# Performance work log

Hardware: AMD Instinct MI355X
Metric: run time of the kernel (lower is better)

Reference implementation:

```python
import jax, jax.numpy as jnp
import numpy as np
import math

D_MODEL = 256
H = 8
D_K = D_MODEL // H
POS_OFFSET = 20
GRID = 7  # module hard-codes key_padding_mask.view(bs, 7, 7)


def _sine_pos_table(num_pos_feats=D_MODEL // 2, temperature=10000, rng=(-20, 20)):
    # faithful port of position_embedding_sine with normalize=True
    scale = 2 * math.pi
    emb = np.arange(rng[0], rng[1] + 1, dtype=np.float32)
    emb = emb / (emb[-1] + 1e-6) * scale  # normalize by last element (=20)
    dim_t = np.arange(num_pos_feats, dtype=np.float32)
    dim_t = temperature ** (2.0 * np.floor(dim_t / 2.0) / num_pos_feats)
    pos = emb[:, None] / dim_t  # [41, 128]
    pos = np.stack((np.sin(pos[:, 0::2]), np.cos(pos[:, 1::2])), axis=-1).reshape(pos.shape[0], -1)
    return jnp.asarray(pos, dtype=jnp.float32)  # [41, 128]


def setup_inputs() -> dict:
    key = jax.random.key(0)
    ks = jax.random.split(key, 8)
    L, B, D = 49, 2048, D_MODEL
    query = jax.random.normal(ks[0], (L, B, D), dtype=jnp.float32)
    key_t = jax.random.normal(ks[1], (L, B, D), dtype=jnp.float32)
    value = jax.random.normal(ks[2], (L, B, D), dtype=jnp.float32)
    key_padding_mask = jnp.zeros((B, L), dtype=bool)  # no padding
    # parameters (xavier-ish init)
    lim = math.sqrt(6.0 / (3 * D + D))
    in_proj_weight = jax.random.uniform(ks[3], (3 * D, D), minval=-lim, maxval=lim, dtype=jnp.float32)
    in_proj_bias = jnp.zeros((3 * D,), dtype=jnp.float32)
    out_w = jax.random.uniform(ks[4], (D, D), minval=-1.0 / math.sqrt(D), maxval=1.0 / math.sqrt(D), dtype=jnp.float32)
    out_b = jnp.zeros((D,), dtype=jnp.float32)
    pos_x = _sine_pos_table()  # [41, 128]
    pos_y = _sine_pos_table()  # [41, 128]
    return {"query": query, "key": key_t, "value": value,
            "key_padding_mask": key_padding_mask,
            "in_proj_weight": in_proj_weight, "in_proj_bias": in_proj_bias,
            "out_w": out_w, "out_b": out_b, "pos_x": pos_x, "pos_y": pos_y}


def reference(query, key, value, key_padding_mask, in_proj_weight, in_proj_bias, out_w, out_b, pos_x, pos_y):
    L, B, D = query.shape
    S = key.shape[0]
    scaling = float(D_K) ** -0.5
    w_q, w_k, w_v = in_proj_weight[:D], in_proj_weight[D:2 * D], in_proj_weight[2 * D:]
    b_q, b_k, b_v = in_proj_bias[:D], in_proj_bias[D:2 * D], in_proj_bias[2 * D:]
    q = (query @ w_q.T + b_q) * scaling          # [L, B, D]
    k = key @ w_k.T + b_k                        # [S, B, D]
    v = value @ w_v.T + b_v                      # [S, B, D]
    # [B, H, L, d_k] etc.
    q4 = q.reshape(L, B, H, D_K).transpose(1, 2, 0, 3)
    k4 = k.reshape(S, B, H, D_K).transpose(1, 2, 0, 3)
    v4 = v.reshape(S, B, H, D_K).transpose(1, 2, 0, 3)
    attn = jnp.einsum('bhld,bhsd->bhls', q4, k4)  # [B, H, L, S]
    # relative position indices from cumsum over the 7x7 grid
    img_mask = (~key_padding_mask).reshape(B, GRID, GRID)
    yy = jnp.cumsum(img_mask.astype(jnp.float32), axis=1).reshape(B, -1)
    xx = jnp.cumsum(img_mask.astype(jnp.float32), axis=2).reshape(B, -1)
    idx_yy = (yy[:, :, None] - yy[:, None, :] + POS_OFFSET).astype(jnp.int32)  # [B, HW, HW]
    idx_xx = (xx[:, :, None] - xx[:, None, :] + POS_OFFSET).astype(jnp.int32)
    # project positional tables through the key weights (faithful slicing)
    k_posy = jnp.einsum('pf,df->pd', pos_y, w_k[:, :D // 2])  # [41, D]
    k_posx = jnp.einsum('pf,df->pd', pos_x, w_k[:, D // 2:])  # [41, D]
    P = k_posy.shape[0]
    k_posy = k_posy.reshape(P, H, D_K)
    k_posx = k_posx.reshape(P, H, D_K)
    posy = jnp.einsum('bhld,phd->bhlp', q4, k_posy)  # [B, H, HW, 41]
    posx = jnp.einsum('bhld,phd->bhlp', q4, k_posx)
    gy = jnp.take_along_axis(posy, jnp.broadcast_to(idx_yy[:, None], posy.shape[:3] + (S,)), axis=-1)
    gx = jnp.take_along_axis(posx, jnp.broadcast_to(idx_xx[:, None], posx.shape[:3] + (S,)), axis=-1)
    attn = attn + gy + gx
    attn = jnp.where(key_padding_mask[:, None, None, :], -jnp.inf, attn)
    attn = jax.nn.softmax(attn, axis=-1)  # dropout skipped (eval mode)
    out = jnp.einsum('bhls,bhsd->bhld', attn, v4)        # [B, H, L, d_k]
    out = out.transpose(2, 0, 1, 3).reshape(L, B, D)     # [L, B, D]
    out = out @ out_w.T + out_b
    return out
```

## Files before the change

### kernel.cpp

```cpp
#include <hip/hip_runtime.h>
#include <hip/hip_bf16.h>

#define L_Q 49
#define D_MODEL 256
#define NHEAD 8
#define DK 32
#define PP 41
#define POS_OFF 20

typedef __attribute__((ext_vector_type(8))) __bf16 bf16x8;
typedef __attribute__((ext_vector_type(4))) float f32x4;
typedef __attribute__((ext_vector_type(8))) unsigned short u16x8;

__device__ __forceinline__ float bf2f(unsigned short u) {
    return __uint_as_float(((unsigned)u) << 16);
}
__device__ __forceinline__ unsigned short f2bf(float f) {
    unsigned u = __float_as_uint(f);
    return (unsigned short)((u + 0x7FFF + ((u >> 16) & 1)) >> 16);
}

__global__ __launch_bounds__(256)
void convert_w(const float* __restrict__ W, const float* __restrict__ out_w,
               float scaling,
               unsigned short* __restrict__ wbf, unsigned short* __restrict__ owbf) {
    int i = blockIdx.x * 256 + threadIdx.x;
    if (i < 49152) {
        int row = i >> 6;
        float sc = (row < 256) ? scaling : 1.0f;
        float4 v = reinterpret_cast<const float4*>(W)[i];
        ushort4 o = { f2bf(v.x * sc), f2bf(v.y * sc), f2bf(v.z * sc), f2bf(v.w * sc) };
        reinterpret_cast<ushort4*>(wbf)[i] = o;
    } else {
        float4 v = reinterpret_cast<const float4*>(out_w)[i - 49152];
        ushort4 o = { f2bf(v.x), f2bf(v.y), f2bf(v.z), f2bf(v.w) };
        reinterpret_cast<ushort4*>(owbf)[i - 49152] = o;
    }
}

__global__ __launch_bounds__(256)
void prep_kpos(const float* __restrict__ pos_y, const float* __restrict__ pos_x,
               const float* __restrict__ W, unsigned short* __restrict__ kpb) {
    int p = blockIdx.x;
    int which = blockIdx.y;
    __shared__ float pr[128];
    int d = threadIdx.x;
    if (d < 128) pr[d] = which ? pos_x[p * 128 + d] : pos_y[p * 128 + d];
    __syncthreads();
    const float* Wk = W + 256 * 256;
    int fOff = which ? 128 : 0;
    float acc = 0.f;
    #pragma unroll 8
    for (int f = 0; f < 128; ++f)
        acc += pr[f] * Wk[(size_t)d * 256 + fOff + f];
    kpb[((size_t)which * PP + p) * 256 + d] = f2bf(acc);
}

__global__ __launch_bounds__(512)
void proj_mfma(const float* __restrict__ Xq, const float* __restrict__ Xk,
               const float* __restrict__ Xv,
               const unsigned short* __restrict__ Wb,
               const float* __restrict__ bias, float scaling,
               unsigned short* __restrict__ outq, unsigned short* __restrict__ outk,
               unsigned short* __restrict__ outv) {
    __shared__ unsigned short Wl[16384];
    __shared__ float Lb[256];
    int which = blockIdx.y;
    int t = blockIdx.x;
    const float* X = (which == 0) ? Xq : ((which == 1) ? Xk : Xv);
    unsigned short* out = (which == 0) ? outq : ((which == 1) ? outk : outv);
    const char* wsrc = (const char*)(Wb + (size_t)which * 65536);

    int tid = threadIdx.x, wid = tid >> 6, lane = tid & 63;
    int rgrp = lane & 15, kgrp = lane >> 4;

    if (tid < 256) Lb[tid] = bias[which * 256 + tid] * ((which == 0) ? scaling : 1.0f);

    size_t row0 = (size_t)t * 256 + wid * 32 + rgrp;
    const float* xp0 = X + row0 * 256 + kgrp * 8;
    const float* xp1 = xp0 + 16 * 256;
    bf16x8 xa[2][8];
    #pragma unroll
    for (int kk = 0; kk < 8; ++kk) {
        float4 a0 = *reinterpret_cast<const float4*>(xp0 + kk * 32);
        float4 a1 = *reinterpret_cast<const float4*>(xp0 + kk * 32 + 4);
        float4 b0 = *reinterpret_cast<const float4*>(xp1 + kk * 32);
        float4 b1 = *reinterpret_cast<const float4*>(xp1 + kk * 32 + 4);
        xa[0][kk][0] = (__bf16)a0.x; xa[0][kk][1] = (__bf16)a0.y;
        xa[0][kk][2] = (__bf16)a0.z; xa[0][kk][3] = (__bf16)a0.w;
        xa[0][kk][4] = (__bf16)a1.x; xa[0][kk][5] = (__bf16)a1.y;
        xa[0][kk][6] = (__bf16)a1.z; xa[0][kk][7] = (__bf16)a1.w;
        xa[1][kk][0] = (__bf16)b0.x; xa[1][kk][1] = (__bf16)b0.y;
        xa[1][kk][2] = (__bf16)b0.z; xa[1][kk][3] = (__bf16)b0.w;
        xa[1][kk][4] = (__bf16)b1.x; xa[1][kk][5] = (__bf16)b1.y;
        xa[1][kk][6] = (__bf16)b1.z; xa[1][kk][7] = (__bf16)b1.w;
    }

    unsigned lbase = ((unsigned)rgrp * 512 + (unsigned)kgrp * 16) ^ ((rgrp & 7) << 4);

    for (int nq = 0; nq < 4; ++nq) {
        if (nq) __syncthreads();
        #pragma unroll
        for (int it = 0; it < 4; ++it) {
            int c = wid + it * 8;
            unsigned dst = (unsigned)c * 1024 + (unsigned)lane * 16;
            unsigned n = dst >> 9;
            unsigned gs = dst ^ ((n & 7) << 4);
            __builtin_amdgcn_global_load_lds(wsrc + nq * 32768 + gs,
                                             (char*)Wl + dst, 16, 0, 0);
        }
        __syncthreads();

        f32x4 acc[2][4];
        #pragma unroll
        for (int m = 0; m < 2; ++m)
            #pragma unroll
            for (int n = 0; n < 4; ++n) acc[m][n] = (f32x4){0.f, 0.f, 0.f, 0.f};

        #pragma unroll
        for (int kk = 0; kk < 8; ++kk) {
            unsigned kb = lbase ^ (unsigned)(kk * 64);
            #pragma unroll
            for (int nt = 0; nt < 4; ++nt) {
                bf16x8 wf = *reinterpret_cast<const bf16x8*>((const char*)Wl + kb + nt * 8192);
                acc[0][nt] = __builtin_amdgcn_mfma_f32_16x16x32_bf16(wf, xa[0][kk], acc[0][nt], 0, 0, 0);
                acc[1][nt] = __builtin_amdgcn_mfma_f32_16x16x32_bf16(wf, xa[1][kk], acc[1][nt], 0, 0, 0);
            }
        }

        #pragma unroll
        for (int mf = 0; mf < 2; ++mf) {
            size_t xrow = row0 + mf * 16;
            #pragma unroll
            for (int nt = 0; nt < 4; ++nt) {
                float4 bv = *reinterpret_cast<const float4*>(&Lb[nq * 64 + nt * 16 + kgrp * 4]);
                ushort4 pk;
                pk.x = f2bf(acc[mf][nt][0] + bv.x);
                pk.y = f2bf(acc[mf][nt][1] + bv.y);
                pk.z = f2bf(acc[mf][nt][2] + bv.z);
                pk.w = f2bf(acc[mf][nt][3] + bv.w);
                *reinterpret_cast<ushort4*>(&out[xrow * 256 + nq * 64 + nt * 16 + kgrp * 4]) = pk;
            }
        }
    }
}

__global__ __launch_bounds__(512)
void out_mfma(const unsigned short* __restrict__ Xb, const unsigned short* __restrict__ Wb,
              const float* __restrict__ bias, float* __restrict__ out) {
    __shared__ unsigned short Wl[16384];
    __shared__ float Lb[256];
    int t = blockIdx.x;
    int tid = threadIdx.x, wid = tid >> 6, lane = tid & 63;
    int rgrp = lane & 15, kgrp = lane >> 4;

    if (tid < 256) Lb[tid] = bias[tid];

    size_t row0 = (size_t)t * 256 + wid * 32 + rgrp;
    const unsigned short* xp0 = Xb + row0 * 256 + kgrp * 8;
    const unsigned short* xp1 = xp0 + 16 * 256;
    bf16x8 xa[2][8];
    #pragma unroll
    for (int kk = 0; kk < 8; ++kk) {
        xa[0][kk] = *reinterpret_cast<const bf16x8*>(xp0 + kk * 32);
        xa[1][kk] = *reinterpret_cast<const bf16x8*>(xp1 + kk * 32);
    }

    unsigned lbase = ((unsigned)rgrp * 512 + (unsigned)kgrp * 16) ^ ((rgrp & 7) << 4);

    for (int nq = 0; nq < 4; ++nq) {
        if (nq) __syncthreads();
        #pragma unroll
        for (int it = 0; it < 4; ++it) {
            int c = wid + it * 8;
            unsigned dst = (unsigned)c * 1024 + (unsigned)lane * 16;
            unsigned n = dst >> 9;
            unsigned gs = dst ^ ((n & 7) << 4);
            __builtin_amdgcn_global_load_lds((const char*)Wb + nq * 32768 + gs,
                                             (char*)Wl + dst, 16, 0, 0);
        }
        __syncthreads();

        f32x4 acc[2][4];
        #pragma unroll
        for (int m = 0; m < 2; ++m)
            #pragma unroll
            for (int n = 0; n < 4; ++n) acc[m][n] = (f32x4){0.f, 0.f, 0.f, 0.f};

        #pragma unroll
        for (int kk = 0; kk < 8; ++kk) {
            unsigned kb = lbase ^ (unsigned)(kk * 64);
            #pragma unroll
            for (int nt = 0; nt < 4; ++nt) {
                bf16x8 wf = *reinterpret_cast<const bf16x8*>((const char*)Wl + kb + nt * 8192);
                acc[0][nt] = __builtin_amdgcn_mfma_f32_16x16x32_bf16(wf, xa[0][kk], acc[0][nt], 0, 0, 0);
                acc[1][nt] = __builtin_amdgcn_mfma_f32_16x16x32_bf16(wf, xa[1][kk], acc[1][nt], 0, 0, 0);
            }
        }

        #pragma unroll
        for (int mf = 0; mf < 2; ++mf) {
            size_t xrow = row0 + mf * 16;
            #pragma unroll
            for (int nt = 0; nt < 4; ++nt) {
                float4 bv = *reinterpret_cast<const float4*>(&Lb[nq * 64 + nt * 16 + kgrp * 4]);
                float4 o;
                o.x = acc[mf][nt][0] + bv.x;
                o.y = acc[mf][nt][1] + bv.y;
                o.z = acc[mf][nt][2] + bv.z;
                o.w = acc[mf][nt][3] + bv.w;
                *reinterpret_cast<float4*>(&out[xrow * 256 + nq * 64 + nt * 16 + kgrp * 4]) = o;
            }
        }
    }
}

__global__ __launch_bounds__(256)
void attn_mfma(const unsigned short* __restrict__ qbuf,
               const unsigned short* __restrict__ kbuf,
               const unsigned short* __restrict__ vbuf,
               const unsigned short* __restrict__ kpb,
               const unsigned char* __restrict__ mask,
               unsigned short* __restrict__ ctx,
               int B) {
    __shared__ unsigned short Kp[96][40];
    __shared__ unsigned short Pt[64][72];
    __shared__ unsigned short Vt[32][72];
    __shared__ unsigned short postab[49][40];
    __shared__ int yy[L_Q], xx[L_Q];
    __shared__ unsigned char mb[52];

    int b = blockIdx.x, h = blockIdx.y;
    int tid = threadIdx.x, wid = tid >> 6, lane = tid & 63;
    int rgrp = lane & 15, kgrp = lane >> 4;
    size_t lstride = (size_t)B * D_MODEL;
    size_t base = (size_t)b * D_MODEL + (size_t)h * DK;

    if (tid < L_Q) mb[tid] = mask[(size_t)b * L_Q + tid];
    if (tid < 196) {
        int l = tid >> 2, c = tid & 3;
        u16x8 vv = *reinterpret_cast<const u16x8*>(vbuf + (size_t)l * lstride + base + c * 8);
        #pragma unroll
        for (int j = 0; j < 8; ++j) Vt[c * 8 + j][l] = vv[j];
    }
    for (int e = tid; e < 512; e += 256) {
        int d = e >> 4, s2 = 48 + (e & 15);
        if (s2 > 48) Vt[d][s2] = 0;
    }
    for (int t = tid; t < 384; t += 256) {
        int r = t >> 2, kc = t & 3;
        const unsigned short* src;
        if (r < 64) {
            int kr = min(r, 48);
            src = kbuf + (size_t)kr * lstride + base + kc * 8;
        } else if (r < 80) {
            int p = r - 64 + 13;
            src = kpb + (size_t)p * D_MODEL + h * DK + kc * 8;
        } else {
            int p = r - 80 + 13;
            src = kpb + (size_t)(PP + p) * D_MODEL + h * DK + kc * 8;
        }
        *reinterpret_cast<u16x8*>(&Kp[r][kc * 8]) = *reinterpret_cast<const u16x8*>(src);
    }
    __syncthreads();
    if (tid < L_Q) {
        int r = tid / 7, c = tid % 7;
        int sy = 0, sx = 0;
        for (int rr = 0; rr <= r; ++rr) sy += (mb[rr * 7 + c] == 0);
        for (int cc = 0; cc <= c; ++cc) sx += (mb[r * 7 + cc] == 0);
        yy[tid] = sy; xx[tid] = sx;
    }
    __syncthreads();

    int qrow = min(16 * wid + rgrp, 48);
    bf16x8 qfrag = *reinterpret_cast<const bf16x8*>(qbuf + (size_t)qrow * lstride + base + kgrp * 8);
    f32x4 acc[6];
    #pragma unroll
    for (int t = 0; t < 6; ++t) {
        bf16x8 bfrag = *reinterpret_cast<const bf16x8*>(&Kp[t * 16 + rgrp][kgrp * 8]);
        acc[t] = __builtin_amdgcn_mfma_f32_16x16x32_bf16(qfrag, bfrag,
                    (f32x4){0.f, 0.f, 0.f, 0.f}, 0, 0, 0);
    }

    #pragma unroll
    for (int i = 0; i < 4; ++i) {
        int l = 16 * wid + kgrp * 4 + i;
        if (l <= 48) {
            postab[l][rgrp]      = f2bf(acc[4][i]);
            postab[l][20 + rgrp] = f2bf(acc[5][i]);
        }
    }
    asm volatile("s_waitcnt lgkmcnt(0)" ::: "memory");

    #pragma unroll
    for (int i = 0; i < 4; ++i) {
        int l = 16 * wid + kgrp * 4 + i;
        int lc = min(l, 48);
        int yyl = yy[lc], xxl = xx[lc];
        float v[4];
        #pragma unroll
        for (int ct = 0; ct < 4; ++ct) {
            int s = ct * 16 + rgrp;
            int sc = min(s, 48);
            int iy = yyl - yy[sc] + (POS_OFF - 13);
            int ix = xxl - xx[sc] + (POS_OFF - 13);
            float val = acc[ct][i] + bf2f(postab[lc][iy]) + bf2f(postab[lc][20 + ix]);
            v[ct] = (s >= L_Q || mb[sc]) ? -1e30f : val;
        }
        float m = fmaxf(fmaxf(v[0], v[1]), fmaxf(v[2], v[3]));
        m = fmaxf(m, __shfl_xor(m, 1));
        m = fmaxf(m, __shfl_xor(m, 2));
        m = fmaxf(m, __shfl_xor(m, 4));
        m = fmaxf(m, __shfl_xor(m, 8));
        float ssum = 0.f, ex[4];
        #pragma unroll
        for (int ct = 0; ct < 4; ++ct) { ex[ct] = __expf(v[ct] - m); ssum += ex[ct]; }
        ssum += __shfl_xor(ssum, 1);
        ssum += __shfl_xor(ssum, 2);
        ssum += __shfl_xor(ssum, 4);
        ssum += __shfl_xor(ssum, 8);
        float is = 1.f / ssum;
        #pragma unroll
        for (int ct = 0; ct < 4; ++ct)
            Pt[l & 63][ct * 16 + rgrp] = f2bf(ex[ct] * is);
    }
    asm volatile("s_waitcnt lgkmcnt(0)" ::: "memory");

    f32x4 oacc[2];
    oacc[0] = (f32x4){0.f, 0.f, 0.f, 0.f};
    oacc[1] = (f32x4){0.f, 0.f, 0.f, 0.f};
    #pragma unroll
    for (int kc = 0; kc < 2; ++kc) {
        bf16x8 pa = *reinterpret_cast<const bf16x8*>(&Pt[16 * wid + rgrp][kc * 32 + kgrp * 8]);
        #pragma unroll
        for (int dt = 0; dt < 2; ++dt) {
            bf16x8 vb = *reinterpret_cast<const bf16x8*>(&Vt[dt * 16 + rgrp][kc * 32 + kgrp * 8]);
            oacc[dt] = __builtin_amdgcn_mfma_f32_16x16x32_bf16(pa, vb, oacc[dt], 0, 0, 0);
        }
    }
    #pragma unroll
    for (int dt = 0; dt < 2; ++dt)
        #pragma unroll
        for (int i = 0; i < 4; ++i) {
            int l = 16 * wid + kgrp * 4 + i;
            if (l <= 48)
                ctx[(size_t)l * lstride + base + dt * 16 + rgrp] = f2bf(oacc[dt][i]);
        }
}

extern "C" void kernel_launch(void* const* d_in, const int* in_sizes, int n_in,
                              void* d_out, int out_size, void* d_ws, size_t ws_size,
                              hipStream_t stream) {
    const float* query = (const float*)d_in[0];
    const float* key   = (const float*)d_in[1];
    const float* value = (const float*)d_in[2];
    const unsigned char* maskp = (const unsigned char*)d_in[3];
    const float* W     = (const float*)d_in[4];
    const float* bias  = (const float*)d_in[5];
    const float* out_w = (const float*)d_in[6];
    const float* out_b = (const float*)d_in[7];
    const float* pos_x = (const float*)d_in[8];
    const float* pos_y = (const float*)d_in[9];
    float* out = (float*)d_out;

    int B = in_sizes[0] / (L_Q * D_MODEL);
    int M = L_Q * B;

    size_t nqkv = (size_t)M * D_MODEL;
    unsigned short* qb = (unsigned short*)d_ws;
    unsigned short* kb = qb + nqkv;
    unsigned short* vb = kb + nqkv;
    unsigned short* kpb = vb + nqkv;
    unsigned short* wbf = kpb + 2 * PP * D_MODEL;
    unsigned short* owbf = wbf + 768 * 256;

    const float scaling = 0.17677669529663687f;

    convert_w<<<256, 256, 0, stream>>>(W, out_w, scaling, wbf, owbf);
    prep_kpos<<<dim3(PP, 2), 256, 0, stream>>>(pos_y, pos_x, W, kpb);

    int gblocks = M / 256;
    proj_mfma<<<dim3(gblocks, 3), 512, 0, stream>>>(query, key, value, wbf, bias, scaling,
                                                    qb, kb, vb);

    attn_mfma<<<dim3(B, NHEAD), 256, 0, stream>>>(qb, kb, vb, kpb, maskp, qb, B);

    out_mfma<<<gblocks, 512, 0, stream>>>(qb, owbf, out_b, out);
}
```

Baseline: 272.3 us.

## Pre-swizzle weights into MFMA fragment order and read directly from global

The weight conversion kernel now writes the bf16 weights in MFMA fragment order, so each lane's 8-element operand is contiguous. The projection and output GEMM kernels then load weight fragments straight from global/L2 and drop the LDS staging, the __syncthreads barriers and the LDS bias copy. This removes LDS traffic and block-wide syncs. In exchange every wave re-reads the weights from cache instead of sharing one LDS copy per block, which raises L2 load pressure.

```diff
diff --git a/kernel.cpp b/kernel.cpp
--- a/kernel.cpp
+++ b/kernel.cpp
@@ -25,17 +25,32 @@
                float scaling,
                unsigned short* __restrict__ wbf, unsigned short* __restrict__ owbf) {
     int i = blockIdx.x * 256 + threadIdx.x;
-    if (i < 49152) {
-        int row = i >> 6;
-        float sc = (row < 256) ? scaling : 1.0f;
-        float4 v = reinterpret_cast<const float4*>(W)[i];
-        ushort4 o = { f2bf(v.x * sc), f2bf(v.y * sc), f2bf(v.z * sc), f2bf(v.w * sc) };
-        reinterpret_cast<ushort4*>(wbf)[i] = o;
+    const float* src;
+    unsigned short* dst;
+    int j, srow_base;
+    float sc = 1.0f;
+    if (i < 24576) {
+        int which = i >> 13;
+        j = i & 8191;
+        src = W; dst = wbf + (size_t)i * 8;
+        srow_base = which * 256;
+        if (which == 0) sc = scaling;
     } else {
-        float4 v = reinterpret_cast<const float4*>(out_w)[i - 49152];
-        ushort4 o = { f2bf(v.x), f2bf(v.y), f2bf(v.z), f2bf(v.w) };
-        reinterpret_cast<ushort4*>(owbf)[i - 49152] = o;
-    }
+        j = i - 24576;
+        src = out_w; dst = owbf + (size_t)j * 8;
+        srow_base = 0;
+    }
+    int nq = j >> 11;
+    int nt = (j >> 9) & 3;
+    int kk = (j >> 6) & 7;
+    int lane = j & 63;
+    int col_local = nq * 64 + nt * 16 + (lane & 15);
+    int k0 = kk * 32 + (lane >> 4) * 8;
+    const float* sp = src + (size_t)(srow_base + col_local) * 256 + k0;
+    unsigned short o[8];
+    #pragma unroll
+    for (int e = 0; e < 8; ++e) o[e] = f2bf(sp[e] * sc);
+    *reinterpret_cast<u16x8*>(dst) = *reinterpret_cast<u16x8*>(o);
 }
 
 __global__ __launch_bounds__(256)
@@ -59,24 +74,20 @@
 __global__ __launch_bounds__(512)
 void proj_mfma(const float* __restrict__ Xq, const float* __restrict__ Xk,
                const float* __restrict__ Xv,
-               const unsigned short* __restrict__ Wb,
+               const unsigned short* __restrict__ Wf,
                const float* __restrict__ bias, float scaling,
                unsigned short* __restrict__ outq, unsigned short* __restrict__ outk,
                unsigned short* __restrict__ outv) {
-    __shared__ unsigned short Wl[16384];
-    __shared__ float Lb[256];
     int which = blockIdx.y;
-    int t = blockIdx.x;
     const float* X = (which == 0) ? Xq : ((which == 1) ? Xk : Xv);
     unsigned short* out = (which == 0) ? outq : ((which == 1) ? outk : outv);
-    const char* wsrc = (const char*)(Wb + (size_t)which * 65536);
+    const unsigned short* wbase = Wf + (size_t)which * 65536;
 
     int tid = threadIdx.x, wid = tid >> 6, lane = tid & 63;
     int rgrp = lane & 15, kgrp = lane >> 4;
-
-    if (tid < 256) Lb[tid] = bias[which * 256 + tid] * ((which == 0) ? scaling : 1.0f);
-
-    size_t row0 = (size_t)t * 256 + wid * 32 + rgrp;
+    float bsc = (which == 0) ? scaling : 1.0f;
+
+    size_t row0 = (size_t)blockIdx.x * 256 + wid * 32 + rgrp;
     const float* xp0 = X + row0 * 256 + kgrp * 8;
     const float* xp1 = xp0 + 16 * 256;
     bf16x8 xa[2][8];
@@ -96,21 +107,8 @@
         xa[1][kk][6] = (__bf16)b1.z; xa[1][kk][7] = (__bf16)b1.w;
     }
 
-    unsigned lbase = ((unsigned)rgrp * 512 + (unsigned)kgrp * 16) ^ ((rgrp & 7) << 4);
-
     for (int nq = 0; nq < 4; ++nq) {
-        if (nq) __syncthreads();
-        #pragma unroll
-        for (int it = 0; it < 4; ++it) {
-            int c = wid + it * 8;
-            unsigned dst = (unsigned)c * 1024 + (unsigned)lane * 16;
-            unsigned n = dst >> 9;
-            unsigned gs = dst ^ ((n & 7) << 4);
-            __builtin_amdgcn_global_load_lds(wsrc + nq * 32768 + gs,
-                                             (char*)Wl + dst, 16, 0, 0);
-        }
-        __syncthreads();
-
+        const unsigned short* wq = wbase + nq * 16384 + lane * 8;
         f32x4 acc[2][4];
         #pragma unroll
         for (int m = 0; m < 2; ++m)
@@ -119,10 +117,9 @@
 
         #pragma unroll
         for (int kk = 0; kk < 8; ++kk) {
-            unsigned kb = lbase ^ (unsigned)(kk * 64);
             #pragma unroll
             for (int nt = 0; nt < 4; ++nt) {
-                bf16x8 wf = *reinterpret_cast<const bf16x8*>((const char*)Wl + kb + nt * 8192);
+                bf16x8 wf = *reinterpret_cast<const bf16x8*>(wq + nt * 4096 + kk * 512);
                 acc[0][nt] = __builtin_amdgcn_mfma_f32_16x16x32_bf16(wf, xa[0][kk], acc[0][nt], 0, 0, 0);
                 acc[1][nt] = __builtin_amdgcn_mfma_f32_16x16x32_bf16(wf, xa[1][kk], acc[1][nt], 0, 0, 0);
             }
@@ -133,30 +130,26 @@
             size_t xrow = row0 + mf * 16;
             #pragma unroll
             for (int nt = 0; nt < 4; ++nt) {
-                float4 bv = *reinterpret_cast<const float4*>(&Lb[nq * 64 + nt * 16 + kgrp * 4]);
+                int col = nq * 64 + nt * 16 + kgrp * 4;
+                float4 bv = *reinterpret_cast<const float4*>(&bias[which * 256 + col]);
                 ushort4 pk;
-                pk.x = f2bf(acc[mf][nt][0] + bv.x);
-                pk.y = f2bf(acc[mf][nt][1] + bv.y);
-                pk.z = f2bf(acc[mf][nt][2] + bv.z);
-                pk.w = f2bf(acc[mf][nt][3] + bv.w);
-                *reinterpret_cast<ushort4*>(&out[xrow * 256 + nq * 64 + nt * 16 + kgrp * 4]) = pk;
+                pk.x = f2bf(acc[mf][nt][0] + bv.x * bsc);
+                pk.y = f2bf(acc[mf][nt][1] + bv.y * bsc);
+                pk.z = f2bf(acc[mf][nt][2] + bv.z * bsc);
+                pk.w = f2bf(acc[mf][nt][3] + bv.w * bsc);
+                *reinterpret_cast<ushort4*>(&out[xrow * 256 + col]) = pk;
             }
         }
     }
 }
 
 __global__ __launch_bounds__(512)
-void out_mfma(const unsigned short* __restrict__ Xb, const unsigned short* __restrict__ Wb,
+void out_mfma(const unsigned short* __restrict__ Xb, const unsigned short* __restrict__ Wf,
               const float* __restrict__ bias, float* __restrict__ out) {
-    __shared__ unsigned short Wl[16384];
-    __shared__ float Lb[256];
-    int t = blockIdx.x;
     int tid = threadIdx.x, wid = tid >> 6, lane = tid & 63;
     int rgrp = lane & 15, kgrp = lane >> 4;
 
-    if (tid < 256) Lb[tid] = bias[tid];
-
-    size_t row0 = (size_t)t * 256 + wid * 32 + rgrp;
+    size_t row0 = (size_t)blockIdx.x * 256 + wid * 32 + rgrp;
     const unsigned short* xp0 = Xb + row0 * 256 + kgrp * 8;
     const unsigned short* xp1 = xp0 + 16 * 256;
     bf16x8 xa[2][8];
@@ -166,21 +159,8 @@
         xa[1][kk] = *reinterpret_cast<const bf16x8*>(xp1 + kk * 32);
     }
 
-    unsigned lbase = ((unsigned)rgrp * 512 + (unsigned)kgrp * 16) ^ ((rgrp & 7) << 4);
-
     for (int nq = 0; nq < 4; ++nq) {
-        if (nq) __syncthreads();
-        #pragma unroll
-        for (int it = 0; it < 4; ++it) {
-            int c = wid + it * 8;
-            unsigned dst = (unsigned)c * 1024 + (unsigned)lane * 16;
-            unsigned n = dst >> 9;
-            unsigned gs = dst ^ ((n & 7) << 4);
-            __builtin_amdgcn_global_load_lds((const char*)Wb + nq * 32768 + gs,
-                                             (char*)Wl + dst, 16, 0, 0);
-        }
-        __syncthreads();
-
+        const unsigned short* wq = Wf + nq * 16384 + lane * 8;
         f32x4 acc[2][4];
         #pragma unroll
         for (int m = 0; m < 2; ++m)
@@ -189,10 +169,9 @@
 
         #pragma unroll
         for (int kk = 0; kk < 8; ++kk) {
-            unsigned kb = lbase ^ (unsigned)(kk * 64);
             #pragma unroll
             for (int nt = 0; nt < 4; ++nt) {
-                bf16x8 wf = *reinterpret_cast<const bf16x8*>((const char*)Wl + kb + nt * 8192);
+                bf16x8 wf = *reinterpret_cast<const bf16x8*>(wq + nt * 4096 + kk * 512);
                 acc[0][nt] = __builtin_amdgcn_mfma_f32_16x16x32_bf16(wf, xa[0][kk], acc[0][nt], 0, 0, 0);
                 acc[1][nt] = __builtin_amdgcn_mfma_f32_16x16x32_bf16(wf, xa[1][kk], acc[1][nt], 0, 0, 0);
             }
@@ -203,13 +182,14 @@
             size_t xrow = row0 + mf * 16;
             #pragma unroll
             for (int nt = 0; nt < 4; ++nt) {
-                float4 bv = *reinterpret_cast<const float4*>(&Lb[nq * 64 + nt * 16 + kgrp * 4]);
+                int col = nq * 64 + nt * 16 + kgrp * 4;
+                float4 bv = *reinterpret_cast<const float4*>(&bias[col]);
                 float4 o;
                 o.x = acc[mf][nt][0] + bv.x;
                 o.y = acc[mf][nt][1] + bv.y;
                 o.z = acc[mf][nt][2] + bv.z;
                 o.w = acc[mf][nt][3] + bv.w;
-                *reinterpret_cast<float4*>(&out[xrow * 256 + nq * 64 + nt * 16 + kgrp * 4]) = o;
+                *reinterpret_cast<float4*>(&out[xrow * 256 + col]) = o;
             }
         }
     }
@@ -376,7 +356,7 @@
 
     const float scaling = 0.17677669529663687f;
 
-    convert_w<<<256, 256, 0, stream>>>(W, out_w, scaling, wbf, owbf);
+    convert_w<<<128, 256, 0, stream>>>(W, out_w, scaling, wbf, owbf);
     prep_kpos<<<dim3(PP, 2), 256, 0, stream>>>(pos_y, pos_x, W, kpb);
 
     int gblocks = M / 256;
```

New measurement: 387.1 us. 42.2% more time.

## Restructure projection GEMMs into double-buffered K-loop with LDS-staged activations

Applied to the files above, without the earlier changes.

Both the QKV projection and output projection kernels are rewritten from a register-resident activation tile with four N-quarter weight passes into a classic 128x256 tile GEMM. The K dimension is walked in 32-wide steps, and both the activation and weight slices are staged into swizzled LDS through async global_load_lds with double buffering. This overlaps memory loads with MFMA work, halves the rows per block, and doubles the grid. The trade-off is more LDS use (64KB in proj_mfma), which may limit occupancy, and fp32 activations are now converted to bf16 from LDS rather than from global loads.

```diff
diff --git a/kernel.cpp b/kernel.cpp
--- a/kernel.cpp
+++ b/kernel.cpp
@@ -63,84 +63,102 @@
                const float* __restrict__ bias, float scaling,
                unsigned short* __restrict__ outq, unsigned short* __restrict__ outk,
                unsigned short* __restrict__ outv) {
-    __shared__ unsigned short Wl[16384];
+    __shared__ unsigned char Sz[65536];
     __shared__ float Lb[256];
     int which = blockIdx.y;
-    int t = blockIdx.x;
     const float* X = (which == 0) ? Xq : ((which == 1) ? Xk : Xv);
     unsigned short* out = (which == 0) ? outq : ((which == 1) ? outk : outv);
     const char* wsrc = (const char*)(Wb + (size_t)which * 65536);
 
     int tid = threadIdx.x, wid = tid >> 6, lane = tid & 63;
     int rgrp = lane & 15, kgrp = lane >> 4;
-
+    int wm = wid & 1, wn = wid >> 1;
+    size_t tile0 = (size_t)blockIdx.x * 128;
+    const char* xsrc = (const char*)X;
+
+    auto stage = [&](int kk, int buf) {
+        #pragma unroll
+        for (int it = 0; it < 2; ++it) {
+            int c = wid + it * 8;
+            {
+                int arow = c * 8 + (lane >> 3);
+                unsigned off = (unsigned)(lane & 7) * 16;
+                unsigned gs = (unsigned)(kk * 128) + (off ^ (((unsigned)arow & 7) << 4));
+                __builtin_amdgcn_global_load_lds(
+                    xsrc + (tile0 + arow) * 1024 + gs,
+                    (char*)Sz + buf * 16384 + c * 1024 + lane * 16, 16, 0, 0);
+            }
+            {
+                int ncol = c * 16 + (lane >> 2);
+                unsigned off = (unsigned)(lane & 3) * 16;
+                unsigned gs = (unsigned)ncol * 512 + (unsigned)(kk * 64)
+                            + (off ^ (((unsigned)ncol & 3) << 4));
+                __builtin_amdgcn_global_load_lds(
+                    wsrc + gs,
+                    (char*)Sz + 32768 + buf * 16384 + c * 1024 + lane * 16, 16, 0, 0);
+            }
+        }
+    };
+
+    stage(0, 0);
     if (tid < 256) Lb[tid] = bias[which * 256 + tid] * ((which == 0) ? scaling : 1.0f);
-
-    size_t row0 = (size_t)t * 256 + wid * 32 + rgrp;
-    const float* xp0 = X + row0 * 256 + kgrp * 8;
-    const float* xp1 = xp0 + 16 * 256;
-    bf16x8 xa[2][8];
-    #pragma unroll
+    __syncthreads();
+
+    f32x4 acc[4][4];
+    #pragma unroll
+    for (int m = 0; m < 4; ++m)
+        #pragma unroll
+        for (int n = 0; n < 4; ++n) acc[m][n] = (f32x4){0.f, 0.f, 0.f, 0.f};
+
+    int buf = 0;
     for (int kk = 0; kk < 8; ++kk) {
-        float4 a0 = *reinterpret_cast<const float4*>(xp0 + kk * 32);
-        float4 a1 = *reinterpret_cast<const float4*>(xp0 + kk * 32 + 4);
-        float4 b0 = *reinterpret_cast<const float4*>(xp1 + kk * 32);
-        float4 b1 = *reinterpret_cast<const float4*>(xp1 + kk * 32 + 4);
-        xa[0][kk][0] = (__bf16)a0.x; xa[0][kk][1] = (__bf16)a0.y;
-        xa[0][kk][2] = (__bf16)a0.z; xa[0][kk][3] = (__bf16)a0.w;
-        xa[0][kk][4] = (__bf16)a1.x; xa[0][kk][5] = (__bf16)a1.y;
-        xa[0][kk][6] = (__bf16)a1.z; xa[0][kk][7] = (__bf16)a1.w;
-        xa[1][kk][0] = (__bf16)b0.x; xa[1][kk][1] = (__bf16)b0.y;
-        xa[1][kk][2] = (__bf16)b0.z; xa[1][kk][3] = (__bf16)b0.w;
-        xa[1][kk][4] = (__bf16)b1.x; xa[1][kk][5] = (__bf16)b1.y;
-        xa[1][kk][6] = (__bf16)b1.z; xa[1][kk][7] = (__bf16)b1.w;
-    }
-
-    unsigned lbase = ((unsigned)rgrp * 512 + (unsigned)kgrp * 16) ^ ((rgrp & 7) << 4);
-
-    for (int nq = 0; nq < 4; ++nq) {
-        if (nq) __syncthreads();
-        #pragma unroll
-        for (int it = 0; it < 4; ++it) {
-            int c = wid + it * 8;
-            unsigned dst = (unsigned)c * 1024 + (unsigned)lane * 16;
-            unsigned n = dst >> 9;
-            unsigned gs = dst ^ ((n & 7) << 4);
-            __builtin_amdgcn_global_load_lds(wsrc + nq * 32768 + gs,
-                                             (char*)Wl + dst, 16, 0, 0);
+        if (kk < 7) stage(kk + 1, buf ^ 1);
+
+        const char* Az = (const char*)Sz + buf * 16384;
+        const char* Bz = (const char*)Sz + 32768 + buf * 16384;
+
+        bf16x8 bf[4];
+        #pragma unroll
+        for (int nt = 0; nt < 4; ++nt) {
+            int ncol = wn * 64 + nt * 16 + rgrp;
+            unsigned ad = (unsigned)ncol * 64
+                        + (((unsigned)kgrp * 16) ^ (((unsigned)ncol & 3) << 4));
+            bf[nt] = *reinterpret_cast<const bf16x8*>(Bz + ad);
+        }
+        #pragma unroll
+        for (int mf = 0; mf < 4; ++mf) {
+            int arow = wm * 64 + mf * 16 + rgrp;
+            unsigned s = ((unsigned)arow & 7) << 4;
+            unsigned a1 = (unsigned)arow * 128 + (((unsigned)kgrp * 32) ^ s);
+            unsigned a2 = (unsigned)arow * 128 + (((unsigned)kgrp * 32 + 16) ^ s);
+            f32x4 q0 = *reinterpret_cast<const f32x4*>(Az + a1);
+            f32x4 q1 = *reinterpret_cast<const f32x4*>(Az + a2);
+            bf16x8 af;
+            af[0] = (__bf16)q0[0]; af[1] = (__bf16)q0[1];
+            af[2] = (__bf16)q0[2]; af[3] = (__bf16)q0[3];
+            af[4] = (__bf16)q1[0]; af[5] = (__bf16)q1[1];
+            af[6] = (__bf16)q1[2]; af[7] = (__bf16)q1[3];
+            #pragma unroll
+            for (int nt = 0; nt < 4; ++nt)
+                acc[mf][nt] = __builtin_amdgcn_mfma_f32_16x16x32_bf16(bf[nt], af, acc[mf][nt], 0, 0, 0);
         }
         __syncthreads();
-
-        f32x4 acc[2][4];
-        #pragma unroll
-        for (int m = 0; m < 2; ++m)
-            #pragma unroll
-            for (int n = 0; n < 4; ++n) acc[m][n] = (f32x4){0.f, 0.f, 0.f, 0.f};
-
-        #pragma unroll
-        for (int kk = 0; kk < 8; ++kk) {
-            unsigned kb = lbase ^ (unsigned)(kk * 64);
-            #pragma unroll
-            for (int nt = 0; nt < 4; ++nt) {
-                bf16x8 wf = *reinterpret_cast<const bf16x8*>((const char*)Wl + kb + nt * 8192);
-                acc[0][nt] = __builtin_amdgcn_mfma_f32_16x16x32_bf16(wf, xa[0][kk], acc[0][nt], 0, 0, 0);
-                acc[1][nt] = __builtin_amdgcn_mfma_f32_16x16x32_bf16(wf, xa[1][kk], acc[1][nt], 0, 0, 0);
-            }
-        }
-
-        #pragma unroll
-        for (int mf = 0; mf < 2; ++mf) {
-            size_t xrow = row0 + mf * 16;
-            #pragma unroll
-            for (int nt = 0; nt < 4; ++nt) {
-                float4 bv = *reinterpret_cast<const float4*>(&Lb[nq * 64 + nt * 16 + kgrp * 4]);
-                ushort4 pk;
-                pk.x = f2bf(acc[mf][nt][0] + bv.x);
-                pk.y = f2bf(acc[mf][nt][1] + bv.y);
-                pk.z = f2bf(acc[mf][nt][2] + bv.z);
-                pk.w = f2bf(acc[mf][nt][3] + bv.w);
-                *reinterpret_cast<ushort4*>(&out[xrow * 256 + nq * 64 + nt * 16 + kgrp * 4]) = pk;
-            }
+        buf ^= 1;
+    }
+
+    #pragma unroll
+    for (int mf = 0; mf < 4; ++mf) {
+        size_t xrow = tile0 + wm * 64 + mf * 16 + rgrp;
+        #pragma unroll
+        for (int nt = 0; nt < 4; ++nt) {
+            int col = wn * 64 + nt * 16 + kgrp * 4;
+            float4 bv = *reinterpret_cast<const float4*>(&Lb[col]);
+            ushort4 pk;
+            pk.x = f2bf(acc[mf][nt][0] + bv.x);
+            pk.y = f2bf(acc[mf][nt][1] + bv.y);
+            pk.z = f2bf(acc[mf][nt][2] + bv.z);
+            pk.w = f2bf(acc[mf][nt][3] + bv.w);
+            *reinterpret_cast<ushort4*>(&out[xrow * 256 + col]) = pk;
         }
     }
 }
@@ -148,69 +166,89 @@
 __global__ __launch_bounds__(512)
 void out_mfma(const unsigned short* __restrict__ Xb, const unsigned short* __restrict__ Wb,
               const float* __restrict__ bias, float* __restrict__ out) {
-    __shared__ unsigned short Wl[16384];
+    __shared__ unsigned char Sz[49152];
     __shared__ float Lb[256];
-    int t = blockIdx.x;
     int tid = threadIdx.x, wid = tid >> 6, lane = tid & 63;
     int rgrp = lane & 15, kgrp = lane >> 4;
-
+    int wm = wid & 1, wn = wid >> 1;
+    size_t tile0 = (size_t)blockIdx.x * 128;
+    const char* xsrc = (const char*)Xb;
+    const char* wsrc = (const char*)Wb;
+
+    auto stage = [&](int kk, int buf) {
+        {
+            int arow = wid * 16 + (lane >> 2);
+            unsigned off = (unsigned)(lane & 3) * 16;
+            unsigned gs = (unsigned)(kk * 64) + (off ^ (((unsigned)arow & 3) << 4));
+            __builtin_amdgcn_global_load_lds(
+                xsrc + (tile0 + arow) * 512 + gs,
+                (char*)Sz + buf * 8192 + wid * 1024 + lane * 16, 16, 0, 0);
+        }
+        #pragma unroll
+        for (int it = 0; it < 2; ++it) {
+            int c = wid + it * 8;
+            int ncol = c * 16 + (lane >> 2);
+            unsigned off = (unsigned)(lane & 3) * 16;
+            unsigned gs = (unsigned)ncol * 512 + (unsigned)(kk * 64)
+                        + (off ^ (((unsigned)ncol & 3) << 4));
+            __builtin_amdgcn_global_load_lds(
+                wsrc + gs,
+                (char*)Sz + 16384 + buf * 16384 + c * 1024 + lane * 16, 16, 0, 0);
+        }
+    };
+
+    stage(0, 0);
     if (tid < 256) Lb[tid] = bias[tid];
-
-    size_t row0 = (size_t)t * 256 + wid * 32 + rgrp;
-    const unsigned short* xp0 = Xb + row0 * 256 + kgrp * 8;
-    const unsigned short* xp1 = xp0 + 16 * 256;
-    bf16x8 xa[2][8];
-    #pragma unroll
+    __syncthreads();
+
+    f32x4 acc[4][4];
+    #pragma unroll
+    for (int m = 0; m < 4; ++m)
+        #pragma unroll
+        for (int n = 0; n < 4; ++n) acc[m][n] = (f32x4){0.f, 0.f, 0.f, 0.f};
+
+    int buf = 0;
     for (int kk = 0; kk < 8; ++kk) {
-        xa[0][kk] = *reinterpret_cast<const bf16x8*>(xp0 + kk * 32);
-        xa[1][kk] = *reinterpret_cast<const bf16x8*>(xp1 + kk * 32);
-    }
-
-    unsigned lbase = ((unsigned)rgrp * 512 + (unsigned)kgrp * 16) ^ ((rgrp & 7) << 4);
-
-    for (int nq = 0; nq < 4; ++nq) {
-        if (nq) __syncthreads();
-        #pragma unroll
-        for (int it = 0; it < 4; ++it) {
-            int c = wid + it * 8;
-            unsigned dst = (unsigned)c * 1024 + (unsigned)lane * 16;
-            unsigned n = dst >> 9;
-            unsigned gs = dst ^ ((n & 7) << 4);
-            __builtin_amdgcn_global_load_lds((const char*)Wb + nq * 32768 + gs,
-                                             (char*)Wl + dst, 16, 0, 0);
+        if (kk < 7) stage(kk + 1, buf ^ 1);
+
+        const char* Az = (const char*)Sz + buf * 8192;
+        const char* Bz = (const char*)Sz + 16384 + buf * 16384;
+
+        bf16x8 bf[4];
+        #pragma unroll
+        for (int nt = 0; nt < 4; ++nt) {
+            int ncol = wn * 64 + nt * 16 + rgrp;
+            unsigned ad = (unsigned)ncol * 64
+                        + (((unsigned)kgrp * 16) ^ (((unsigned)ncol & 3) << 4));
+            bf[nt] = *reinterpret_cast<const bf16x8*>(Bz + ad);
+        }
+        #pragma unroll
+        for (int mf = 0; mf < 4; ++mf) {
+            int arow = wm * 64 + mf * 16 + rgrp;
+            unsigned ad = (unsigned)arow * 64
+                        + (((unsigned)kgrp * 16) ^ (((unsigned)arow & 3) << 4));
+            bf16x8 af = *reinterpret_cast<const bf16x8*>(Az + ad);
+            #pragma unroll
+            for (int nt = 0; nt < 4; ++nt)
+                acc[mf][nt] = __builtin_amdgcn_mfma_f32_16x16x32_bf16(bf[nt], af, acc[mf][nt], 0, 0, 0);
         }
         __syncthreads();
-
-        f32x4 acc[2][4];
-        #pragma unroll
-        for (int m = 0; m < 2; ++m)
-            #pragma unroll
-            for (int n = 0; n < 4; ++n) acc[m][n] = (f32x4){0.f, 0.f, 0.f, 0.f};
-
-        #pragma unroll
-        for (int kk = 0; kk < 8; ++kk) {
-            unsigned kb = lbase ^ (unsigned)(kk * 64);
-            #pragma unroll
-            for (int nt = 0; nt < 4; ++nt) {
-                bf16x8 wf = *reinterpret_cast<const bf16x8*>((const char*)Wl + kb + nt * 8192);
-                acc[0][nt] = __builtin_amdgcn_mfma_f32_16x16x32_bf16(wf, xa[0][kk], acc[0][nt], 0, 0, 0);
-                acc[1][nt] = __builtin_amdgcn_mfma_f32_16x16x32_bf16(wf, xa[1][kk], acc[1][nt], 0, 0, 0);
-            }
-        }
-
-        #pragma unroll
-        for (int mf = 0; mf < 2; ++mf) {
-            size_t xrow = row0 + mf * 16;
-            #pragma unroll
-            for (int nt = 0; nt < 4; ++nt) {
-                float4 bv = *reinterpret_cast<const float4*>(&Lb[nq * 64 + nt * 16 + kgrp * 4]);
-                float4 o;
-                o.x = acc[mf][nt][0] + bv.x;
-                o.y = acc[mf][nt][1] + bv.y;
-                o.z = acc[mf][nt][2] + bv.z;
-                o.w = acc[mf][nt][3] + bv.w;
-                *reinterpret_cast<float4*>(&out[xrow * 256 + nq * 64 + nt * 16 + kgrp * 4]) = o;
-            }
+        buf ^= 1;
+    }
+
+    #pragma unroll
+    for (int mf = 0; mf < 4; ++mf) {
+        size_t xrow = tile0 + wm * 64 + mf * 16 + rgrp;
+        #pragma unroll
+        for (int nt = 0; nt < 4; ++nt) {
+            int col = wn * 64 + nt * 16 + kgrp * 4;
+            float4 bv = *reinterpret_cast<const float4*>(&Lb[col]);
+            float4 o;
+            o.x = acc[mf][nt][0] + bv.x;
+            o.y = acc[mf][nt][1] + bv.y;
+            o.z = acc[mf][nt][2] + bv.z;
+            o.w = acc[mf][nt][3] + bv.w;
+            *reinterpret_cast<float4*>(&out[xrow * 256 + col]) = o;
         }
     }
 }
@@ -379,11 +417,11 @@
     convert_w<<<256, 256, 0, stream>>>(W, out_w, scaling, wbf, owbf);
     prep_kpos<<<dim3(PP, 2), 256, 0, stream>>>(pos_y, pos_x, W, kpb);
 
-    int gblocks = M / 256;
-    proj_mfma<<<dim3(gblocks, 3), 512, 0, stream>>>(query, key, value, wbf, bias, scaling,
-                                                    qb, kb, vb);
+    int tiles = M / 128;
+    proj_mfma<<<dim3(tiles, 3), 512, 0, stream>>>(query, key, value, wbf, bias, scaling,
+                                                  qb, kb, vb);
 
     attn_mfma<<<dim3(B, NHEAD), 256, 0, stream>>>(qb, kb, vb, kpb, maskp, qb, B);
 
-    out_mfma<<<gblocks, 512, 0, stream>>>(qb, owbf, out_b, out);
-}
+    out_mfma<<<tiles, 512, 0, stream>>>(qb, owbf, out_b, out);
+}
```

After: 274.4 us. No clear change (+0.8%).
